# Kernel tuning notes

Hardware: AMD Instinct MI355X
Metric: run time of the kernel (lower is better)

The kernel has to match this reference:

```python
import jax, jax.numpy as jnp
import numpy as np

D_MODEL = 1024
N_HEADS = 16
HEAD_DIM = D_MODEL // N_HEADS
NEG_INF = -1e10  # masked_fill value used in the original


def setup_inputs() -> dict:
    key = jax.random.key(0)
    ks = jax.random.split(key, 12)
    B, L = 2, 2048
    s = 0.02
    return {
        "query": jax.random.normal(ks[0], (B, L, D_MODEL), jnp.float32),
        "key": jax.random.normal(ks[1], (B, L, D_MODEL), jnp.float32),
        "value": jax.random.normal(ks[2], (B, L, D_MODEL), jnp.float32),
        "mask": jnp.ones((B, 1, L, L), jnp.int32),
        "Wq": jax.random.normal(ks[3], (D_MODEL, D_MODEL), jnp.float32) * s,
        "bq": jax.random.normal(ks[4], (D_MODEL,), jnp.float32) * s,
        "Wk": jax.random.normal(ks[5], (D_MODEL, D_MODEL), jnp.float32) * s,
        "bk": jax.random.normal(ks[6], (D_MODEL,), jnp.float32) * s,
        "Wv": jax.random.normal(ks[7], (D_MODEL, D_MODEL), jnp.float32) * s,
        "bv": jax.random.normal(ks[8], (D_MODEL,), jnp.float32) * s,
        "Wo": jax.random.normal(ks[9], (D_MODEL, D_MODEL), jnp.float32) * s,
        "bo": jax.random.normal(ks[10], (D_MODEL,), jnp.float32) * s,
    }


def _split_heads(x, B):
    # [B, L, D] -> [B, H, L, hd]
    return x.reshape(B, -1, N_HEADS, HEAD_DIM).transpose(0, 2, 1, 3)


def reference(query, key, value, mask, Wq, bq, Wk, bk, Wv, bv, Wo, bo):
    B = query.shape[0]
    scale = jnp.sqrt(jnp.asarray(HEAD_DIM, query.dtype))
    Q = _split_heads(query @ Wq + bq, B)   # [B,H,Lq,hd]
    K = _split_heads(key @ Wk + bk, B)     # [B,H,Lk,hd]
    V = _split_heads(value @ Wv + bv, B)   # [B,H,Lk,hd]
    energy = jnp.einsum('bhqd,bhkd->bhqk', Q, K) / scale
    energy = jnp.where(mask == 0, jnp.asarray(NEG_INF, energy.dtype), energy)
    # NOTE: the original applies softmax over dim=1 (the HEADS axis); replicated faithfully.
    attention = jax.nn.softmax(energy, axis=1)
    x = jnp.einsum('bhqk,bhkd->bhqd', attention, V)  # dropout is identity at inference
    x = x.transpose(0, 2, 1, 3).reshape(B, -1, D_MODEL)
    return x @ Wo + bo
```

## Files before the change

### kernel.cpp

```cpp
#include <hip/hip_runtime.h>
#include <hip/hip_bf16.h>
#include <stdint.h>

#define DM 1024
#define NH 16
#define HD 64
#define SEQ 2048
#define NB 2
#define NC 4
#define KCH (SEQ / NC)

typedef __attribute__((ext_vector_type(8)))  __bf16 bf16x8;
typedef __attribute__((ext_vector_type(4)))  __bf16 bf16x4;
typedef __attribute__((ext_vector_type(4)))  float  f32x4;
typedef __attribute__((ext_vector_type(16))) float  f32x16;
typedef __attribute__((ext_vector_type(4)))  unsigned int uint4v;
typedef __attribute__((ext_vector_type(4)))  int    i32x4;

__device__ __forceinline__ f32x16 mfma32x32(bf16x8 a, bf16x8 b, f32x16 c) {
  return __builtin_amdgcn_mfma_f32_32x32x16_bf16(a, b, c, 0, 0, 0);
}
__device__ __forceinline__ f32x4 mfma16x16(bf16x8 a, bf16x8 b, f32x4 c) {
  return __builtin_amdgcn_mfma_f32_16x16x32_bf16(a, b, c, 0, 0, 0);
}
__device__ __forceinline__ unsigned pkbf(float a, float b) {
  unsigned short ua = __builtin_bit_cast(unsigned short, (__bf16)a);
  unsigned short ub = __builtin_bit_cast(unsigned short, (__bf16)b);
  return (unsigned)ua | ((unsigned)ub << 16);
}
__device__ __forceinline__ f32x16 zero16() {
  f32x16 z;
#pragma unroll
  for (int i = 0; i < 16; i++) z[i] = 0.0f;
  return z;
}

__global__ void wconv_kernel(const float* __restrict__ Wq, const float* __restrict__ Wk,
                             const float* __restrict__ Wv, const float* __restrict__ Wo,
                             __bf16* __restrict__ Wt) {
  __shared__ float tile[32][33];
  const int which = blockIdx.z;
  const float* W = (which == 0) ? Wq : (which == 1) ? Wk : (which == 2) ? Wv : Wo;
  __bf16* out = Wt + (size_t)which * DM * DM;
  const int n0 = blockIdx.x * 32, k0 = blockIdx.y * 32;
  const int tx = threadIdx.x & 31, ty = threadIdx.x >> 5;
#pragma unroll
  for (int i = 0; i < 4; i++) {
    tile[ty + i * 8][tx] = W[(size_t)(k0 + ty + i * 8) * DM + n0 + tx];
  }
  __syncthreads();
#pragma unroll
  for (int i = 0; i < 4; i++) {
    out[(size_t)(n0 + ty + i * 8) * DM + k0 + tx] = (__bf16)tile[tx][ty + i * 8];
  }
}

__global__ __launch_bounds__(256, 3)
void qkv_kernel(const float* __restrict__ Aq, const float* __restrict__ Ak,
                const float* __restrict__ Av, const __bf16* __restrict__ Wt,
                const float* __restrict__ bqv, const float* __restrict__ bkv,
                const float* __restrict__ bvv, __bf16* __restrict__ Qh,
                __bf16* __restrict__ Kh, __bf16* __restrict__ Vt) {
  __shared__ __bf16 Alds[128][40];
  __shared__ __bf16 Blds[128][40];
  const int z = blockIdx.z;
  const float* A = (z == 0) ? Aq : (z == 1) ? Ak : Av;
  const __bf16* Bt = Wt + (size_t)z * DM * DM;
  const float* bias = (z == 0) ? bqv : (z == 1) ? bkv : bvv;

  const int tid = threadIdx.x;
  const int l = tid & 63, w = tid >> 6;
  const int wm = w >> 1, wn = w & 1;
  const int r0 = blockIdx.x * 128, c0 = blockIdx.y * 128;

  f32x4 acc[4][4];
#pragma unroll
  for (int m = 0; m < 4; m++)
#pragma unroll
    for (int n = 0; n < 4; n++)
#pragma unroll
      for (int r = 0; r < 4; r++) acc[m][n][r] = 0.0f;

  const int ar = tid >> 2;
  const int aq = tid & 3;
  const int br = tid >> 1;
  const int bh = tid & 1;

  for (int kt = 0; kt < DM / 32; kt++) {
#pragma unroll
    for (int rep = 0; rep < 2; rep++) {
      const int row = ar + rep * 64;
      const float* src = A + (size_t)(r0 + row) * DM + kt * 32 + aq * 8;
      const f32x4 v0 = *(const f32x4*)(src);
      const f32x4 v1 = *(const f32x4*)(src + 4);
      bf16x8 av;
#pragma unroll
      for (int i = 0; i < 4; i++) { av[i] = (__bf16)v0[i]; av[4 + i] = (__bf16)v1[i]; }
      *(bf16x8*)&Alds[row][aq * 8] = av;
    }
    {
      const __bf16* bsrc = Bt + (size_t)(c0 + br) * DM + kt * 32 + bh * 16;
      bf16x8 v0 = *(const bf16x8*)bsrc;
      bf16x8 v1 = *(const bf16x8*)(bsrc + 8);
      *(bf16x8*)&Blds[br][bh * 16] = v0;
      *(bf16x8*)&Blds[br][bh * 16 + 8] = v1;
    }
    __syncthreads();
    bf16x8 af[4], bfr[4];
#pragma unroll
    for (int m = 0; m < 4; m++)
      af[m] = *(const bf16x8*)&Alds[wm * 64 + m * 16 + (l & 15)][(l >> 4) * 8];
#pragma unroll
    for (int n = 0; n < 4; n++)
      bfr[n] = *(const bf16x8*)&Blds[wn * 64 + n * 16 + (l & 15)][(l >> 4) * 8];
#pragma unroll
    for (int m = 0; m < 4; m++)
#pragma unroll
      for (int n = 0; n < 4; n++) acc[m][n] = mfma16x16(af[m], bfr[n], acc[m][n]);
    __syncthreads();
  }

  const int ccol = l & 15;
  const int crb = (l >> 4) * 4;
  __bf16* Ohm = (z == 0) ? Qh : Kh;
#pragma unroll
  for (int n = 0; n < 4; n++) {
    const int col = c0 + wn * 64 + n * 16 + ccol;
    const float bv = bias[col];
    const int h = col >> 6, d = col & 63;
#pragma unroll
    for (int m = 0; m < 4; m++) {
      const int row = r0 + wm * 64 + m * 16 + crb;
      f32x4 v = acc[m][n];
#pragma unroll
      for (int r = 0; r < 4; r++) v[r] += bv;
      if (z < 2) {
#pragma unroll
        for (int r = 0; r < 4; r++) {
          const int rr = row + r; const int bb = rr >> 11; const int ll = rr & 2047;
          Ohm[(((size_t)bb * NH + h) * SEQ + ll) * HD + d] = (__bf16)v[r];
        }
      } else {
        const int bb = row >> 11, ll = row & 2047;
        bf16x4 pk;
#pragma unroll
        for (int r = 0; r < 4; r++) pk[r] = (__bf16)v[r];
        *(bf16x4*)&Vt[(((size_t)bb * NH + h) * HD + d) * SEQ + ll] = pk;
      }
    }
  }
}

__device__ __forceinline__ void process_head(const float (&pp)[16], const float (&rd)[16],
                                             int hi, int lq, int k0,
                                             const __bf16* __restrict__ vbase,
                                             f32x16& x0, f32x16& x1) {
  unsigned u[8];
#pragma unroll
  for (int j = 0; j < 8; j++) {
    const float a = pp[2 * j] * rd[2 * j];
    const float b = pp[2 * j + 1] * rd[2 * j + 1];
    u[j] = pkbf(a, b);
  }
  unsigned t[8];
#pragma unroll
  for (int j = 0; j < 8; j++) t[j] = (unsigned)__shfl_xor((int)u[j], 32, 64);
  const unsigned w0 = hi ? t[2] : u[0];
  const unsigned w1 = hi ? t[3] : u[1];
  const unsigned w2 = hi ? u[2] : t[0];
  const unsigned w3 = hi ? u[3] : t[1];
  const unsigned w4 = hi ? t[6] : u[4];
  const unsigned w5 = hi ? t[7] : u[5];
  const unsigned w6 = hi ? u[6] : t[4];
  const unsigned w7 = hi ? u[7] : t[5];
  const uint4v s0v = {w0, w1, w2, w3};
  const uint4v s1v = {w4, w5, w6, w7};
  const bf16x8 pa0 = __builtin_bit_cast(bf16x8, s0v);
  const bf16x8 pa1 = __builtin_bit_cast(bf16x8, s1v);
  const __bf16* vp = vbase + (size_t)lq * SEQ + k0 + hi * 8;
  bf16x8 vf;
  vf = *(const bf16x8*)(vp);                         x0 = mfma32x32(pa0, vf, x0);
  vf = *(const bf16x8*)(vp + 16);                    x0 = mfma32x32(pa1, vf, x0);
  vf = *(const bf16x8*)(vp + (size_t)32 * SEQ);      x1 = mfma32x32(pa0, vf, x1);
  vf = *(const bf16x8*)(vp + (size_t)32 * SEQ + 16); x1 = mfma32x32(pa1, vf, x1);
}

__global__ __launch_bounds__(512, 4)
void attn_kernel(const __bf16* __restrict__ Qh, const __bf16* __restrict__ Kh,
                 const __bf16* __restrict__ Vt, const int* __restrict__ mask,
                 __bf16* __restrict__ Xp) {
  __shared__ float part[8 * 64 * 16];
  __shared__ float Dbuf[1024];
  __shared__ unsigned mbits[32 * 17];
  const int tid = threadIdx.x;
  const int l = tid & 63;
  const int w = tid >> 6;
  const int lq = l & 31;
  const int hi = l >> 5;
  const int qt = blockIdx.x, b = blockIdx.y, c = blockIdx.z;
  const int q0 = qt * 32;
  const int h0 = w * 2;

  {
    const int qq = tid >> 4, wi = tid & 15;
    const i32x4* mp = (const i32x4*)(mask + ((size_t)b * SEQ + q0 + qq) * SEQ +
                                     (size_t)c * KCH + wi * 32);
    unsigned word = 0;
#pragma unroll
    for (int j = 0; j < 8; j++) {
      const i32x4 v = mp[j];
      word |= (v.x ? 1u : 0u) << (4 * j);
      word |= (v.y ? 1u : 0u) << (4 * j + 1);
      word |= (v.z ? 1u : 0u) << (4 * j + 2);
      word |= (v.w ? 1u : 0u) << (4 * j + 3);
    }
    mbits[qq * 17 + wi] = word;
  }

  bf16x8 qf[2][4];
#pragma unroll
  for (int hh = 0; hh < 2; hh++) {
    const __bf16* qp = Qh + (((size_t)b * NH + h0 + hh) * SEQ + q0 + lq) * HD + hi * 8;
#pragma unroll
    for (int ch = 0; ch < 4; ch++) qf[hh][ch] = *(const bf16x8*)(qp + ch * 16);
  }
  f32x16 xacc[2][2];
#pragma unroll
  for (int i = 0; i < 2; i++)
#pragma unroll
    for (int j = 0; j < 2; j++) xacc[i][j] = zero16();

  const __bf16* kbase0 = Kh + ((size_t)b * NH + h0) * SEQ * HD;
  const __bf16* kbase1 = Kh + ((size_t)b * NH + h0 + 1) * SEQ * HD;
  const __bf16* vbase0 = Vt + ((size_t)b * NH + h0) * HD * SEQ;
  const __bf16* vbase1 = Vt + ((size_t)b * NH + h0 + 1) * HD * SEQ;

  __syncthreads();

  for (int kt = 0; kt < KCH / 32; kt++) {
    const int k0 = c * KCH + kt * 32;

    f32x16 e0 = zero16(), e1 = zero16();
#pragma unroll
    for (int ch = 0; ch < 4; ch++) {
      const bf16x8 kf = *(const bf16x8*)(kbase0 + ((size_t)(k0 + lq)) * HD + ch * 16 + hi * 8);
      e0 = mfma32x32(kf, qf[0][ch], e0);
    }
#pragma unroll
    for (int ch = 0; ch < 4; ch++) {
      const bf16x8 kf = *(const bf16x8*)(kbase1 + ((size_t)(k0 + lq)) * HD + ch * 16 + hi * 8);
      e1 = mfma32x32(kf, qf[1][ch], e1);
    }
    const unsigned mword = mbits[lq * 17 + kt];
    float p0[16], p1[16], s4[16];
#pragma unroll
    for (int r = 0; r < 16; r++) {
      const int crow = (r & 3) + 8 * (r >> 2) + 4 * hi;
      const float bv = ((mword >> crow) & 1u) ? 0.0f : -1e10f;
      const float a0 = fmaf(e0[r], 0.125f, bv);
      const float a1 = fmaf(e1[r], 0.125f, bv);
      p0[r] = __expf(a0);
      p1[r] = __expf(a1);
      s4[r] = p0[r] + p1[r];
    }
    {
      float* pw = &part[(unsigned)((w << 6) | l) * 16];
#pragma unroll
      for (int i = 0; i < 4; i++) {
        f32x4 v;
#pragma unroll
        for (int j = 0; j < 4; j++) v[j] = s4[4 * i + j];
        *(f32x4*)(pw + 4 * i) = v;
      }
    }
    __syncthreads();
    {
      const int p2 = tid * 2;
      float da = 0.0f, db = 0.0f;
#pragma unroll
      for (int w2 = 0; w2 < 8; w2++) {
        da += part[w2 * 1024 + p2];
        db += part[w2 * 1024 + p2 + 1];
      }
      Dbuf[p2] = da;
      Dbuf[p2 + 1] = db;
    }
    __syncthreads();
    float rd[16];
#pragma unroll
    for (int i = 0; i < 4; i++) {
      const f32x4 dv = *(const f32x4*)&Dbuf[l * 16 + i * 4];
#pragma unroll
      for (int j = 0; j < 4; j++) rd[4 * i + j] = __builtin_amdgcn_rcpf(dv[j]);
    }
    process_head(p0, rd, hi, lq, k0, vbase0, xacc[0][0], xacc[0][1]);
    process_head(p1, rd, hi, lq, k0, vbase1, xacc[1][0], xacc[1][1]);
  }

  const size_t XCH = (size_t)NB * NH * SEQ * HD;
#pragma unroll
  for (int hh = 0; hh < 2; hh++) {
    __bf16* xo = Xp + (size_t)c * XCH +
                 (((size_t)b * NH + h0 + hh) * SEQ + q0) * HD;
#pragma unroll
    for (int dt = 0; dt < 2; dt++) {
#pragma unroll
      for (int r = 0; r < 16; r++) {
        const int crow = (r & 3) + 8 * (r >> 2) + 4 * hi;
        xo[(size_t)crow * HD + dt * 32 + lq] = (__bf16)xacc[hh][dt][r];
      }
    }
  }
}

__global__ __launch_bounds__(256, 4)
void ogemm_kernel(const __bf16* __restrict__ Xp, const __bf16* __restrict__ Bt,
                  const float* __restrict__ bias, float* __restrict__ Out) {
  __shared__ __bf16 Alds[64][40];
  __shared__ __bf16 Blds[128][40];
  const int tid = threadIdx.x;
  const int l = tid & 63, w = tid >> 6;
  const int r0 = blockIdx.x * 64, c0 = blockIdx.y * 128;

  f32x4 acc[4][2];
#pragma unroll
  for (int m = 0; m < 4; m++)
#pragma unroll
    for (int n = 0; n < 2; n++)
#pragma unroll
      for (int r = 0; r < 4; r++) acc[m][n][r] = 0.0f;

  const int ar = tid >> 2, aq = tid & 3;
  const int br = tid >> 1, bh = tid & 1;
  const size_t PART = (size_t)NB * NH * SEQ * HD;
  const int rr = r0 + ar;
  const int bb = rr >> 11, ll = rr & 2047;

  for (int kt = 0; kt < DM / 32; kt++) {
    {
      const int cc = kt * 32 + aq * 8;
      const int h = cc >> 6, d = cc & 63;
      const size_t off = (((size_t)bb * NH + h) * SEQ + ll) * HD + d;
      float fv[8];
#pragma unroll
      for (int i = 0; i < 8; i++) fv[i] = 0.0f;
#pragma unroll
      for (int c = 0; c < NC; c++) {
        const bf16x8 v = *(const bf16x8*)(Xp + (size_t)c * PART + off);
#pragma unroll
        for (int i = 0; i < 8; i++) fv[i] += (float)v[i];
      }
      bf16x8 av;
#pragma unroll
      for (int i = 0; i < 8; i++) av[i] = (__bf16)fv[i];
      *(bf16x8*)&Alds[ar][aq * 8] = av;
    }
    {
      const __bf16* bsrc = Bt + (size_t)(c0 + br) * DM + kt * 32 + bh * 16;
      bf16x8 v0 = *(const bf16x8*)bsrc;
      bf16x8 v1 = *(const bf16x8*)(bsrc + 8);
      *(bf16x8*)&Blds[br][bh * 16] = v0;
      *(bf16x8*)&Blds[br][bh * 16 + 8] = v1;
    }
    __syncthreads();
    bf16x8 af[4], bfr[2];
#pragma unroll
    for (int m = 0; m < 4; m++)
      af[m] = *(const bf16x8*)&Alds[m * 16 + (l & 15)][(l >> 4) * 8];
#pragma unroll
    for (int n = 0; n < 2; n++)
      bfr[n] = *(const bf16x8*)&Blds[w * 32 + n * 16 + (l & 15)][(l >> 4) * 8];
#pragma unroll
    for (int m = 0; m < 4; m++)
#pragma unroll
      for (int n = 0; n < 2; n++) acc[m][n] = mfma16x16(af[m], bfr[n], acc[m][n]);
    __syncthreads();
  }

  const int ccol = l & 15;
  const int crb = (l >> 4) * 4;
#pragma unroll
  for (int n = 0; n < 2; n++) {
    const int col = c0 + w * 32 + n * 16 + ccol;
    const float bv = bias[col];
#pragma unroll
    for (int m = 0; m < 4; m++) {
      const int row = r0 + m * 16 + crb;
      f32x4 v = acc[m][n];
#pragma unroll
      for (int r = 0; r < 4; r++) Out[(size_t)(row + r) * DM + col] = v[r] + bv;
    }
  }
}

extern "C" void kernel_launch(void* const* d_in, const int* in_sizes, int n_in,
                              void* d_out, int out_size, void* d_ws, size_t ws_size,
                              hipStream_t stream) {
  const float* q = (const float*)d_in[0];
  const float* k = (const float*)d_in[1];
  const float* v = (const float*)d_in[2];
  const int* msk = (const int*)d_in[3];
  const float* Wq = (const float*)d_in[4];
  const float* bq = (const float*)d_in[5];
  const float* Wk = (const float*)d_in[6];
  const float* bk = (const float*)d_in[7];
  const float* Wv = (const float*)d_in[8];
  const float* bv = (const float*)d_in[9];
  const float* Wo = (const float*)d_in[10];
  const float* bo = (const float*)d_in[11];

  char* ws = (char*)d_ws;
  const size_t MB = 1024 * 1024;
  if (ws_size < 64 * MB) return;
  __bf16* Wt = (__bf16*)(ws);
  __bf16* Qh = (__bf16*)(ws + 8 * MB);
  __bf16* Kh = (__bf16*)(ws + 16 * MB);
  __bf16* Vt = (__bf16*)(ws + 24 * MB);
  __bf16* Xp = (__bf16*)(ws + 32 * MB);

  wconv_kernel<<<dim3(32, 32, 4), 256, 0, stream>>>(Wq, Wk, Wv, Wo, Wt);
  qkv_kernel<<<dim3(32, 8, 3), 256, 0, stream>>>(q, k, v, Wt, bq, bk, bv, Qh, Kh, Vt);
  attn_kernel<<<dim3(64, 2, NC), 512, 0, stream>>>(Qh, Kh, Vt, msk, Xp);
  ogemm_kernel<<<dim3(64, 8), 256, 0, stream>>>(Xp, Wt + (size_t)3 * DM * DM, bo, (float*)d_out);
}
```

Measured before the change: 518.8 us.

## Split head-axis softmax into separate denominator pass and per-head attention kernel

```diff
diff --git a/kernel.cpp b/kernel.cpp
--- a/kernel.cpp
+++ b/kernel.cpp
@@ -7,8 +7,6 @@
 #define HD 64
 #define SEQ 2048
 #define NB 2
-#define NC 4
-#define KCH (SEQ / NC)
 
 typedef __attribute__((ext_vector_type(8)))  __bf16 bf16x8;
 typedef __attribute__((ext_vector_type(4)))  __bf16 bf16x4;
@@ -151,61 +149,22 @@
   }
 }
 
-__device__ __forceinline__ void process_head(const float (&pp)[16], const float (&rd)[16],
-                                             int hi, int lq, int k0,
-                                             const __bf16* __restrict__ vbase,
-                                             f32x16& x0, f32x16& x1) {
-  unsigned u[8];
-#pragma unroll
-  for (int j = 0; j < 8; j++) {
-    const float a = pp[2 * j] * rd[2 * j];
-    const float b = pp[2 * j + 1] * rd[2 * j + 1];
-    u[j] = pkbf(a, b);
-  }
-  unsigned t[8];
-#pragma unroll
-  for (int j = 0; j < 8; j++) t[j] = (unsigned)__shfl_xor((int)u[j], 32, 64);
-  const unsigned w0 = hi ? t[2] : u[0];
-  const unsigned w1 = hi ? t[3] : u[1];
-  const unsigned w2 = hi ? u[2] : t[0];
-  const unsigned w3 = hi ? u[3] : t[1];
-  const unsigned w4 = hi ? t[6] : u[4];
-  const unsigned w5 = hi ? t[7] : u[5];
-  const unsigned w6 = hi ? u[6] : t[4];
-  const unsigned w7 = hi ? u[7] : t[5];
-  const uint4v s0v = {w0, w1, w2, w3};
-  const uint4v s1v = {w4, w5, w6, w7};
-  const bf16x8 pa0 = __builtin_bit_cast(bf16x8, s0v);
-  const bf16x8 pa1 = __builtin_bit_cast(bf16x8, s1v);
-  const __bf16* vp = vbase + (size_t)lq * SEQ + k0 + hi * 8;
-  bf16x8 vf;
-  vf = *(const bf16x8*)(vp);                         x0 = mfma32x32(pa0, vf, x0);
-  vf = *(const bf16x8*)(vp + 16);                    x0 = mfma32x32(pa1, vf, x0);
-  vf = *(const bf16x8*)(vp + (size_t)32 * SEQ);      x1 = mfma32x32(pa0, vf, x1);
-  vf = *(const bf16x8*)(vp + (size_t)32 * SEQ + 16); x1 = mfma32x32(pa1, vf, x1);
-}
-
-__global__ __launch_bounds__(512, 4)
-void attn_kernel(const __bf16* __restrict__ Qh, const __bf16* __restrict__ Kh,
-                 const __bf16* __restrict__ Vt, const int* __restrict__ mask,
-                 __bf16* __restrict__ Xp) {
-  __shared__ float part[8 * 64 * 16];
-  __shared__ float Dbuf[1024];
-  __shared__ unsigned mbits[32 * 17];
+__global__ __launch_bounds__(512, 2)
+void denom_kernel(const __bf16* __restrict__ Qh, const __bf16* __restrict__ Kh,
+                  const int* __restrict__ mask, __bf16* __restrict__ Dinv,
+                  unsigned* __restrict__ mbit) {
   const int tid = threadIdx.x;
-  const int l = tid & 63;
-  const int w = tid >> 6;
-  const int lq = l & 31;
-  const int hi = l >> 5;
-  const int qt = blockIdx.x, b = blockIdx.y, c = blockIdx.z;
+  const int l = tid & 63, w = tid >> 6;
+  const int lq = l & 31, hi = l >> 5;
+  const int ktg = blockIdx.x;
+  const int b = blockIdx.y;
+  const int qt = blockIdx.z;
   const int q0 = qt * 32;
-  const int h0 = w * 2;
-
+  const int k0 = (ktg * 8 + w) * 32;
+
+  unsigned word = 0;
   {
-    const int qq = tid >> 4, wi = tid & 15;
-    const i32x4* mp = (const i32x4*)(mask + ((size_t)b * SEQ + q0 + qq) * SEQ +
-                                     (size_t)c * KCH + wi * 32);
-    unsigned word = 0;
+    const i32x4* mp = (const i32x4*)(mask + ((size_t)b * SEQ + q0 + lq) * SEQ + k0);
 #pragma unroll
     for (int j = 0; j < 8; j++) {
       const i32x4 v = mp[j];
@@ -214,107 +173,128 @@
       word |= (v.z ? 1u : 0u) << (4 * j + 2);
       word |= (v.w ? 1u : 0u) << (4 * j + 3);
     }
-    mbits[qq * 17 + wi] = word;
-  }
-
-  bf16x8 qf[2][4];
-#pragma unroll
-  for (int hh = 0; hh < 2; hh++) {
-    const __bf16* qp = Qh + (((size_t)b * NH + h0 + hh) * SEQ + q0 + lq) * HD + hi * 8;
-#pragma unroll
-    for (int ch = 0; ch < 4; ch++) qf[hh][ch] = *(const bf16x8*)(qp + ch * 16);
-  }
-  f32x16 xacc[2][2];
-#pragma unroll
-  for (int i = 0; i < 2; i++)
-#pragma unroll
-    for (int j = 0; j < 2; j++) xacc[i][j] = zero16();
-
-  const __bf16* kbase0 = Kh + ((size_t)b * NH + h0) * SEQ * HD;
-  const __bf16* kbase1 = Kh + ((size_t)b * NH + h0 + 1) * SEQ * HD;
-  const __bf16* vbase0 = Vt + ((size_t)b * NH + h0) * HD * SEQ;
-  const __bf16* vbase1 = Vt + ((size_t)b * NH + h0 + 1) * HD * SEQ;
-
-  __syncthreads();
-
-  for (int kt = 0; kt < KCH / 32; kt++) {
-    const int k0 = c * KCH + kt * 32;
-
-    f32x16 e0 = zero16(), e1 = zero16();
+    if (hi == 0) mbit[((size_t)b * SEQ + q0 + lq) * (SEQ / 32) + (k0 >> 5)] = word;
+  }
+
+  float dsum[16];
+#pragma unroll
+  for (int r = 0; r < 16; r++) dsum[r] = 0.0f;
+
+  const __bf16* qbase = Qh + ((size_t)b * NH) * SEQ * HD + (size_t)(q0 + lq) * HD + hi * 8;
+  const __bf16* kbase = Kh + ((size_t)b * NH) * SEQ * HD + (size_t)(k0 + lq) * HD + hi * 8;
+
+  for (int h = 0; h < NH; h++) {
+    const __bf16* qp = qbase + (size_t)h * SEQ * HD;
+    const __bf16* kp = kbase + (size_t)h * SEQ * HD;
+    bf16x8 qf[4], kf[4];
 #pragma unroll
     for (int ch = 0; ch < 4; ch++) {
-      const bf16x8 kf = *(const bf16x8*)(kbase0 + ((size_t)(k0 + lq)) * HD + ch * 16 + hi * 8);
-      e0 = mfma32x32(kf, qf[0][ch], e0);
-    }
-#pragma unroll
-    for (int ch = 0; ch < 4; ch++) {
-      const bf16x8 kf = *(const bf16x8*)(kbase1 + ((size_t)(k0 + lq)) * HD + ch * 16 + hi * 8);
-      e1 = mfma32x32(kf, qf[1][ch], e1);
-    }
-    const unsigned mword = mbits[lq * 17 + kt];
-    float p0[16], p1[16], s4[16];
+      qf[ch] = *(const bf16x8*)(qp + ch * 16);
+      kf[ch] = *(const bf16x8*)(kp + ch * 16);
+    }
+    f32x16 e = zero16();
+#pragma unroll
+    for (int ch = 0; ch < 4; ch++) e = mfma32x32(kf[ch], qf[ch], e);
 #pragma unroll
     for (int r = 0; r < 16; r++) {
       const int crow = (r & 3) + 8 * (r >> 2) + 4 * hi;
-      const float bv = ((mword >> crow) & 1u) ? 0.0f : -1e10f;
-      const float a0 = fmaf(e0[r], 0.125f, bv);
-      const float a1 = fmaf(e1[r], 0.125f, bv);
-      p0[r] = __expf(a0);
-      p1[r] = __expf(a1);
-      s4[r] = p0[r] + p1[r];
-    }
-    {
-      float* pw = &part[(unsigned)((w << 6) | l) * 16];
-#pragma unroll
-      for (int i = 0; i < 4; i++) {
-        f32x4 v;
-#pragma unroll
-        for (int j = 0; j < 4; j++) v[j] = s4[4 * i + j];
-        *(f32x4*)(pw + 4 * i) = v;
-      }
-    }
-    __syncthreads();
-    {
-      const int p2 = tid * 2;
-      float da = 0.0f, db = 0.0f;
-#pragma unroll
-      for (int w2 = 0; w2 < 8; w2++) {
-        da += part[w2 * 1024 + p2];
-        db += part[w2 * 1024 + p2 + 1];
-      }
-      Dbuf[p2] = da;
-      Dbuf[p2 + 1] = db;
-    }
-    __syncthreads();
-    float rd[16];
-#pragma unroll
-    for (int i = 0; i < 4; i++) {
-      const f32x4 dv = *(const f32x4*)&Dbuf[l * 16 + i * 4];
-#pragma unroll
-      for (int j = 0; j < 4; j++) rd[4 * i + j] = __builtin_amdgcn_rcpf(dv[j]);
-    }
-    process_head(p0, rd, hi, lq, k0, vbase0, xacc[0][0], xacc[0][1]);
-    process_head(p1, rd, hi, lq, k0, vbase1, xacc[1][0], xacc[1][1]);
-  }
-
-  const size_t XCH = (size_t)NB * NH * SEQ * HD;
-#pragma unroll
-  for (int hh = 0; hh < 2; hh++) {
-    __bf16* xo = Xp + (size_t)c * XCH +
-                 (((size_t)b * NH + h0 + hh) * SEQ + q0) * HD;
-#pragma unroll
-    for (int dt = 0; dt < 2; dt++) {
-#pragma unroll
-      for (int r = 0; r < 16; r++) {
-        const int crow = (r & 3) + 8 * (r >> 2) + 4 * hi;
-        xo[(size_t)crow * HD + dt * 32 + lq] = (__bf16)xacc[hh][dt][r];
-      }
+      const float bv = ((word >> crow) & 1u) ? 0.0f : -1e10f;
+      dsum[r] += __expf(fmaf(e[r], 0.125f, bv));
+    }
+  }
+#pragma unroll
+  for (int r = 0; r < 16; r++) {
+    const int crow = (r & 3) + 8 * (r >> 2) + 4 * hi;
+    Dinv[((size_t)b * SEQ + k0 + crow) * SEQ + q0 + lq] =
+        (__bf16)__builtin_amdgcn_rcpf(dsum[r]);
+  }
+}
+
+__global__ __launch_bounds__(256, 2)
+void attn2_kernel(const __bf16* __restrict__ Qh, const __bf16* __restrict__ Kh,
+                  const __bf16* __restrict__ Vt, const __bf16* __restrict__ Dinv,
+                  const unsigned* __restrict__ mbit, __bf16* __restrict__ X) {
+  const int tid = threadIdx.x;
+  const int l = tid & 63, w = tid >> 6;
+  const int lq = l & 31, hi = l >> 5;
+  const int bh = blockIdx.x;
+  const int b = bh >> 4;
+  const int q0 = (blockIdx.y * 4 + w) * 32;
+
+  bf16x8 qf[4];
+  {
+    const __bf16* qp = Qh + ((size_t)bh * SEQ + q0 + lq) * HD + hi * 8;
+#pragma unroll
+    for (int ch = 0; ch < 4; ch++) qf[ch] = *(const bf16x8*)(qp + ch * 16);
+  }
+  f32x16 x0 = zero16(), x1 = zero16();
+
+  const __bf16* kbase = Kh + (size_t)bh * SEQ * HD;
+  const __bf16* vbase = Vt + (size_t)bh * HD * SEQ;
+  const unsigned* mrow = mbit + ((size_t)b * SEQ + q0 + lq) * (SEQ / 32);
+  const __bf16* drow = Dinv + (size_t)b * SEQ * SEQ + q0 + lq;
+
+  for (int kt = 0; kt < SEQ / 32; kt++) {
+    const int k0 = kt * 32;
+    f32x16 e = zero16();
+#pragma unroll
+    for (int ch = 0; ch < 4; ch++) {
+      const bf16x8 kf = *(const bf16x8*)(kbase + (size_t)(k0 + lq) * HD + ch * 16 + hi * 8);
+      e = mfma32x32(kf, qf[ch], e);
+    }
+    const unsigned word = mrow[kt];
+    float p[16], rd[16];
+#pragma unroll
+    for (int r = 0; r < 16; r++) {
+      const int crow = (r & 3) + 8 * (r >> 2) + 4 * hi;
+      const float bv = ((word >> crow) & 1u) ? 0.0f : -1e10f;
+      p[r] = __expf(fmaf(e[r], 0.125f, bv));
+      rd[r] = (float)drow[(size_t)(k0 + crow) * SEQ];
+    }
+    unsigned u[8];
+#pragma unroll
+    for (int j = 0; j < 8; j++) {
+      const float a = p[2 * j] * rd[2 * j];
+      const float bb2 = p[2 * j + 1] * rd[2 * j + 1];
+      u[j] = pkbf(a, bb2);
+    }
+    unsigned t[8];
+#pragma unroll
+    for (int j = 0; j < 8; j++) t[j] = (unsigned)__shfl_xor((int)u[j], 32, 64);
+    const unsigned w0 = hi ? t[2] : u[0];
+    const unsigned w1 = hi ? t[3] : u[1];
+    const unsigned w2 = hi ? u[2] : t[0];
+    const unsigned w3 = hi ? u[3] : t[1];
+    const unsigned w4 = hi ? t[6] : u[4];
+    const unsigned w5 = hi ? t[7] : u[5];
+    const unsigned w6 = hi ? u[6] : t[4];
+    const unsigned w7 = hi ? u[7] : t[5];
+    const uint4v s0v = {w0, w1, w2, w3};
+    const uint4v s1v = {w4, w5, w6, w7};
+    const bf16x8 pa0 = __builtin_bit_cast(bf16x8, s0v);
+    const bf16x8 pa1 = __builtin_bit_cast(bf16x8, s1v);
+    const __bf16* vp = vbase + (size_t)lq * SEQ + k0 + hi * 8;
+    bf16x8 vf;
+    vf = *(const bf16x8*)(vp);                         x0 = mfma32x32(pa0, vf, x0);
+    vf = *(const bf16x8*)(vp + 16);                    x0 = mfma32x32(pa1, vf, x0);
+    vf = *(const bf16x8*)(vp + (size_t)32 * SEQ);      x1 = mfma32x32(pa0, vf, x1);
+    vf = *(const bf16x8*)(vp + (size_t)32 * SEQ + 16); x1 = mfma32x32(pa1, vf, x1);
+  }
+
+  __bf16* xo = X + ((size_t)bh * SEQ + q0) * HD;
+#pragma unroll
+  for (int dt = 0; dt < 2; dt++) {
+    const f32x16& xx = dt ? x1 : x0;
+#pragma unroll
+    for (int r = 0; r < 16; r++) {
+      const int crow = (r & 3) + 8 * (r >> 2) + 4 * hi;
+      xo[(size_t)crow * HD + dt * 32 + lq] = (__bf16)xx[r];
     }
   }
 }
 
 __global__ __launch_bounds__(256, 4)
-void ogemm_kernel(const __bf16* __restrict__ Xp, const __bf16* __restrict__ Bt,
+void ogemm_kernel(const __bf16* __restrict__ X, const __bf16* __restrict__ Bt,
                   const float* __restrict__ bias, float* __restrict__ Out) {
   __shared__ __bf16 Alds[64][40];
   __shared__ __bf16 Blds[128][40];
@@ -332,7 +312,6 @@
 
   const int ar = tid >> 2, aq = tid & 3;
   const int br = tid >> 1, bh = tid & 1;
-  const size_t PART = (size_t)NB * NH * SEQ * HD;
   const int rr = r0 + ar;
   const int bb = rr >> 11, ll = rr & 2047;
 
@@ -341,19 +320,7 @@
       const int cc = kt * 32 + aq * 8;
       const int h = cc >> 6, d = cc & 63;
       const size_t off = (((size_t)bb * NH + h) * SEQ + ll) * HD + d;
-      float fv[8];
-#pragma unroll
-      for (int i = 0; i < 8; i++) fv[i] = 0.0f;
-#pragma unroll
-      for (int c = 0; c < NC; c++) {
-        const bf16x8 v = *(const bf16x8*)(Xp + (size_t)c * PART + off);
-#pragma unroll
-        for (int i = 0; i < 8; i++) fv[i] += (float)v[i];
-      }
-      bf16x8 av;
-#pragma unroll
-      for (int i = 0; i < 8; i++) av[i] = (__bf16)fv[i];
-      *(bf16x8*)&Alds[ar][aq * 8] = av;
+      *(bf16x8*)&Alds[ar][aq * 8] = *(const bf16x8*)(X + off);
     }
     {
       const __bf16* bsrc = Bt + (size_t)(c0 + br) * DM + kt * 32 + bh * 16;
@@ -416,10 +383,13 @@
   __bf16* Qh = (__bf16*)(ws + 8 * MB);
   __bf16* Kh = (__bf16*)(ws + 16 * MB);
   __bf16* Vt = (__bf16*)(ws + 24 * MB);
-  __bf16* Xp = (__bf16*)(ws + 32 * MB);
+  __bf16* X  = (__bf16*)(ws + 32 * MB);
+  __bf16* Dinv = (__bf16*)(ws + 40 * MB);
+  unsigned* mbit = (unsigned*)(ws + 57 * MB);
 
   wconv_kernel<<<dim3(32, 32, 4), 256, 0, stream>>>(Wq, Wk, Wv, Wo, Wt);
   qkv_kernel<<<dim3(32, 8, 3), 256, 0, stream>>>(q, k, v, Wt, bq, bk, bv, Qh, Kh, Vt);
-  attn_kernel<<<dim3(64, 2, NC), 512, 0, stream>>>(Qh, Kh, Vt, msk, Xp);
-  ogemm_kernel<<<dim3(64, 8), 256, 0, stream>>>(Xp, Wt + (size_t)3 * DM * DM, bo, (float*)d_out);
-}
+  denom_kernel<<<dim3(8, 2, 64), 512, 0, stream>>>(Qh, Kh, msk, Dinv, mbit);
+  attn2_kernel<<<dim3(32, 16), 256, 0, stream>>>(Qh, Kh, Vt, Dinv, mbit, X);
+  ogemm_kernel<<<dim3(64, 8), 256, 0, stream>>>(X, Wt + (size_t)3 * DM * DM, bo, (float*)d_out);
+}
```

After: 511.3 us. About the same (-1.4%).
